# Optimization experiments

Measured on AMD Instinct MI355X. Metric: run time of the kernel, lower is better.

## Reference

```python
import jax, jax.numpy as jnp
import numpy as np

D_MODEL = 1024
N_HEADS = 16
HIDDEN = 256
PER_HEAD = 256
EPS = 1e-6


def setup_inputs() -> dict:
    key = jax.random.key(0)
    ks = jax.random.split(key, 6)
    B = 1024
    x = jax.random.normal(ks[0], (B, 64, D_MODEL), dtype=jnp.float32)
    # token_compress: Linear(d_model, 32, bias=False) -> weight (32, d_model)
    W_tc = jax.random.normal(ks[1], (32, D_MODEL), dtype=jnp.float32) / np.sqrt(D_MODEL)
    # global_compress: Linear(64*32, hidden) with bias, then RMSNorm(hidden)
    W_gc = jax.random.normal(ks[2], (HIDDEN, 64 * 32), dtype=jnp.float32) / np.sqrt(64 * 32)
    b_gc = jnp.zeros((HIDDEN,), dtype=jnp.float32)
    rms_scale = jnp.ones((HIDDEN,), dtype=jnp.float32)
    # per-head projections stacked: (n_heads, per_head, hidden)
    W_heads = jax.random.normal(ks[3], (N_HEADS, PER_HEAD, HIDDEN), dtype=jnp.float32) / np.sqrt(HIDDEN)
    # attn_logit_proj: Linear(per_head, 64*64, bias=False) -> (4096, per_head)
    W_logit = jax.random.normal(ks[4], (64 * 64, PER_HEAD), dtype=jnp.float32) / np.sqrt(PER_HEAD)
    return {"x": x, "W_tc": W_tc, "W_gc": W_gc, "b_gc": b_gc,
            "rms_scale": rms_scale, "W_heads": W_heads, "W_logit": W_logit}


def reference(x, W_tc, W_gc, b_gc, rms_scale, W_heads, W_logit):
    B = x.shape[0]
    # token compress: (B, 64, d_model) -> (B, 64, 32)
    compressed = jnp.einsum('bsd,kd->bsk', x, W_tc)
    flat = compressed.reshape(B, 64 * 32)
    # global compress + RMSNorm
    g = flat @ W_gc.T + b_gc                      # (B, hidden)
    rms = jnp.sqrt(jnp.mean(g * g, axis=-1, keepdims=True) + EPS)
    g = g / rms * rms_scale
    # batched per-head projection: (B, n_heads, per_head)
    head_repr = jnp.einsum('bh,nph->bnp', g, W_heads)
    # shared attn logit projection: (B, n_heads, 4096)
    logits = jnp.einsum('bnp,qp->bnq', head_repr, W_logit)
    return logits.reshape(B, N_HEADS, 64, 64)
```

## Files before the change

### kernel.cpp

```cpp
#include <hip/hip_runtime.h>


typedef unsigned short ushort_t;
typedef __attribute__((ext_vector_type(8))) short bf16x8;
typedef __attribute__((ext_vector_type(4))) float f32x4;
typedef __attribute__((ext_vector_type(4))) unsigned int u32x4;
typedef __attribute__((ext_vector_type(2))) unsigned int u32x2;

#define MFMA16(a, b, c) __builtin_amdgcn_mfma_f32_16x16x32_bf16((a), (b), (c), 0, 0, 0)

__device__ __forceinline__ unsigned bfround(float f) {
  unsigned u = __builtin_bit_cast(unsigned, f);
  return u + 0x7fffu + ((u >> 16) & 1u);
}
__device__ __forceinline__ unsigned pack2(float lo, float hi) {
  return (bfround(lo) >> 16) | (bfround(hi) & 0xffff0000u);
}

__device__ __forceinline__ void gld16(const ushort_t* g, ushort_t* l) {
  __builtin_amdgcn_global_load_lds(
      (const __attribute__((address_space(1))) unsigned int*)g,
      (__attribute__((address_space(3))) unsigned int*)l, 16, 0, 0);
}

__global__ __launch_bounds__(256) void k_cvt(const float* __restrict__ Wtc,
                                             const float* __restrict__ Wgc,
                                             const float* __restrict__ Wh,
                                             const float* __restrict__ Wl,
                                             ushort_t* __restrict__ oTc,
                                             ushort_t* __restrict__ oGc,
                                             ushort_t* __restrict__ oWh,
                                             ushort_t* __restrict__ oWl) {
  size_t g = (size_t)blockIdx.x * 256 + threadIdx.x;
  const float* src; ushort_t* dst; size_t off;
  if (g < 4096)        { src = Wtc; dst = oTc; off = g; }
  else if (g < 69632)  { src = Wgc; dst = oGc; off = g - 4096; }
  else if (g < 200704) { src = Wh;  dst = oWh; off = g - 69632; }
  else                 { src = Wl;  dst = oWl; off = g - 200704; }
  float4 f0 = ((const float4*)src)[off * 2];
  float4 f1 = ((const float4*)src)[off * 2 + 1];
  u32x4 p;
  p.x = pack2(f0.x, f0.y); p.y = pack2(f0.z, f0.w);
  p.z = pack2(f1.x, f1.y); p.w = pack2(f1.z, f1.w);
  ((u32x4*)dst)[off] = p;
}

__global__ __launch_bounds__(256) void k_tok(const float* __restrict__ x,
                                             const ushort_t* __restrict__ WtcBf,
                                             ushort_t* __restrict__ flatBf) {
  __shared__ ushort_t lb[32][264];
  const int t = threadIdx.x;
  const int w = t >> 6, l = t & 63, col16 = l & 15, quad = l >> 4;
  const float* arow = x + (size_t)blockIdx.x * 65536 + (size_t)(w * 16 + col16) * 1024;
  f32x4 acc0 = {0.f, 0.f, 0.f, 0.f}, acc1 = {0.f, 0.f, 0.f, 0.f};

  for (int ko = 0; ko < 1024; ko += 256) {
    float4 af[16];
#pragma unroll
    for (int s = 0; s < 8; ++s) {
      af[2 * s]     = *(const float4*)(arow + ko + s * 32 + quad * 8);
      af[2 * s + 1] = *(const float4*)(arow + ko + s * 32 + quad * 8 + 4);
    }
    __syncthreads();
    {
      int r = t >> 3, c0 = (t & 7) * 32;
      const ushort_t* src = WtcBf + (size_t)r * 1024 + ko + c0;
#pragma unroll
      for (int c = 0; c < 4; ++c)
        *(bf16x8*)&lb[r][c0 + c * 8] = *(const bf16x8*)(src + c * 8);
    }
    __syncthreads();
#pragma unroll
    for (int s = 0; s < 8; ++s) {
      u32x4 p;
      p.x = pack2(af[2 * s].x, af[2 * s].y);
      p.y = pack2(af[2 * s].z, af[2 * s].w);
      p.z = pack2(af[2 * s + 1].x, af[2 * s + 1].y);
      p.w = pack2(af[2 * s + 1].z, af[2 * s + 1].w);
      bf16x8 a = __builtin_bit_cast(bf16x8, p);
      bf16x8 b0 = *(const bf16x8*)&lb[col16][s * 32 + quad * 8];
      bf16x8 b1 = *(const bf16x8*)&lb[16 + col16][s * 32 + quad * 8];
      acc0 = MFMA16(b0, a, acc0);
      acc1 = MFMA16(b1, a, acc1);
    }
  }
  ushort_t* ob = flatBf + (size_t)blockIdx.x * 2048;
  const int m = w * 16 + col16;
  u32x2 v0, v1;
  v0.x = pack2(acc0[0], acc0[1]); v0.y = pack2(acc0[2], acc0[3]);
  v1.x = pack2(acc1[0], acc1[1]); v1.y = pack2(acc1[2], acc1[3]);
  *(u32x2*)&ob[m * 32 + quad * 4] = v0;
  *(u32x2*)&ob[m * 32 + 16 + quad * 4] = v1;
}

__global__ __launch_bounds__(256) void k_gc_part(const ushort_t* __restrict__ Abf,
                                                 const ushort_t* __restrict__ Bbf,
                                                 float* __restrict__ Hpart) {
  __shared__ ushort_t la[16][40];
  __shared__ ushort_t lb[256][40];
  const int t = threadIdx.x;
  const int w = t >> 6, l = t & 63, col16 = l & 15, quad = l >> 4;
  const int b0 = blockIdx.x * 16;
  const int k0 = blockIdx.y * 512;
  f32x4 acc[4];
#pragma unroll
  for (int j = 0; j < 4; ++j) acc[j] = (f32x4){0.f, 0.f, 0.f, 0.f};

  for (int kk = 0; kk < 512; kk += 32) {
    __syncthreads();
    if (t < 128) {
      int r = t >> 3, c0 = (t & 7) * 4;
      *(ushort4*)&la[r][c0] =
          *(const ushort4*)(Abf + (size_t)(b0 + r) * 2048 + k0 + kk + c0);
    }
    {
      const ushort_t* src = Bbf + (size_t)t * 2048 + k0 + kk;
#pragma unroll
      for (int c = 0; c < 4; ++c)
        *(bf16x8*)&lb[t][c * 8] = *(const bf16x8*)(src + c * 8);
    }
    __syncthreads();
    bf16x8 af = *(const bf16x8*)&la[col16][quad * 8];
#pragma unroll
    for (int j = 0; j < 4; ++j) {
      bf16x8 bfj = *(const bf16x8*)&lb[w * 64 + j * 16 + col16][quad * 8];
      acc[j] = MFMA16(bfj, af, acc[j]);
    }
  }
  float* o = Hpart + (size_t)blockIdx.y * 262144;
#pragma unroll
  for (int j = 0; j < 4; ++j)
    *(f32x4*)&o[(size_t)(b0 + col16) * 256 + w * 64 + j * 16 + quad * 4] = acc[j];
}

__global__ __launch_bounds__(256) void k_gc_red(const float* __restrict__ Hpart,
                                                const float* __restrict__ bias,
                                                const float* __restrict__ rscale,
                                                ushort_t* __restrict__ gBf) {
  __shared__ float lred[16][17];
  __shared__ float linv[16];
  const int t = threadIdx.x;
  const int row = t >> 4, seg = t & 15;
  const size_t base = (size_t)(blockIdx.x * 16 + row) * 256 + seg * 16;
  float v[16];
#pragma unroll
  for (int k = 0; k < 4; ++k) {
    float4 s0 = *(const float4*)(Hpart + base + k * 4);
    float4 s1 = *(const float4*)(Hpart + 262144 + base + k * 4);
    float4 s2 = *(const float4*)(Hpart + 524288 + base + k * 4);
    float4 s3 = *(const float4*)(Hpart + 786432 + base + k * 4);
    float4 bi = *(const float4*)(bias + seg * 16 + k * 4);
    v[k * 4 + 0] = s0.x + s1.x + s2.x + s3.x + bi.x;
    v[k * 4 + 1] = s0.y + s1.y + s2.y + s3.y + bi.y;
    v[k * 4 + 2] = s0.z + s1.z + s2.z + s3.z + bi.z;
    v[k * 4 + 3] = s0.w + s1.w + s2.w + s3.w + bi.w;
  }
  float ss = 0.f;
#pragma unroll
  for (int k = 0; k < 16; ++k) ss += v[k] * v[k];
  lred[row][seg] = ss;
  __syncthreads();
  if (t < 16) {
    float s = 0.f;
#pragma unroll
    for (int k = 0; k < 16; ++k) s += lred[t][k];
    linv[t] = 1.0f / sqrtf(s * (1.0f / 256.0f) + 1e-6f);
  }
  __syncthreads();
  float iv = linv[row];
  float rs[16];
#pragma unroll
  for (int k = 0; k < 4; ++k)
    *(float4*)&rs[k * 4] = *(const float4*)(rscale + seg * 16 + k * 4);
  u32x4 p0, p1;
  p0.x = pack2(v[0] * iv * rs[0],  v[1] * iv * rs[1]);
  p0.y = pack2(v[2] * iv * rs[2],  v[3] * iv * rs[3]);
  p0.z = pack2(v[4] * iv * rs[4],  v[5] * iv * rs[5]);
  p0.w = pack2(v[6] * iv * rs[6],  v[7] * iv * rs[7]);
  p1.x = pack2(v[8] * iv * rs[8],  v[9] * iv * rs[9]);
  p1.y = pack2(v[10] * iv * rs[10], v[11] * iv * rs[11]);
  p1.z = pack2(v[12] * iv * rs[12], v[13] * iv * rs[13]);
  p1.w = pack2(v[14] * iv * rs[14], v[15] * iv * rs[15]);
  *(u32x4*)(gBf + base) = p0;
  *(u32x4*)(gBf + base + 8) = p1;
}

template <bool OBF>
__global__ __launch_bounds__(256) void k_gemm(const ushort_t* __restrict__ A,
                                              const ushort_t* __restrict__ Bw,
                                              float* __restrict__ Cf,
                                              ushort_t* __restrict__ Cb) {
  __shared__ ushort_t la[2][4096];
  __shared__ ushort_t lb[2][4096];
  const int t = threadIdx.x;
  const int w = t >> 6, l = t & 63, col16 = l & 15, quad = l >> 4;
  const int wm = w >> 1, wn = w & 1;
  const int id = blockIdx.x;
  const int id2 = (id & 7) * ((int)gridDim.x >> 3) + (id >> 3);
  const size_t am0 = (size_t)(id2 >> 5) * 128;
  const size_t bn0 = (size_t)(id2 & 31) * 128;

  f32x4 acc[4][4];
#pragma unroll
  for (int i = 0; i < 4; ++i)
#pragma unroll
    for (int j = 0; j < 4; ++j) acc[i][j] = (f32x4){0.f, 0.f, 0.f, 0.f};

  auto STAGE = [&](int buf, int kk) {
#pragma unroll
    for (int i = 0; i < 2; ++i) {
      int L = i * 256 + t;
      int r = L >> 2;
      int cs = (L & 3) ^ (r & 3);
      ushort_t* da = &la[buf][(size_t)(i * 256 + (w << 6)) * 8];
      ushort_t* db = &lb[buf][(size_t)(i * 256 + (w << 6)) * 8];
      gld16(A + (am0 + r) * 256 + kk + cs * 8, da);
      gld16(Bw + (bn0 + r) * 256 + kk + cs * 8, db);
    }
  };

  STAGE(0, 0);
  __syncthreads();
#pragma unroll
  for (int tix = 0; tix < 8; ++tix) {
    const int buf = tix & 1;
    if (tix < 7) STAGE(buf ^ 1, (tix + 1) * 32);
    bf16x8 af[4], bfv[4];
#pragma unroll
    for (int i = 0; i < 4; ++i) {
      int R = wm * 64 + i * 16 + col16;
      af[i] = *(const bf16x8*)&la[buf][(size_t)((R << 2) + (quad ^ (R & 3))) * 8];
    }
#pragma unroll
    for (int j = 0; j < 4; ++j) {
      int R = wn * 64 + j * 16 + col16;
      bfv[j] = *(const bf16x8*)&lb[buf][(size_t)((R << 2) + (quad ^ (R & 3))) * 8];
    }
#pragma unroll
    for (int i = 0; i < 4; ++i)
#pragma unroll
      for (int j = 0; j < 4; ++j)
        acc[i][j] = MFMA16(bfv[j], af[i], acc[i][j]);
    __syncthreads();
  }

#pragma unroll
  for (int i = 0; i < 4; ++i)
#pragma unroll
    for (int j = 0; j < 4; ++j) {
      size_t row = am0 + wm * 64 + i * 16 + col16;
      size_t cc = bn0 + wn * 64 + j * 16 + quad * 4;
      if (OBF) {
        u32x2 v;
        v.x = pack2(acc[i][j][0], acc[i][j][1]);
        v.y = pack2(acc[i][j][2], acc[i][j][3]);
        *(u32x2*)&Cb[row * 4096 + cc] = v;
      } else {
        *(f32x4*)&Cf[row * 4096 + cc] = acc[i][j];
      }
    }
}

extern "C" void kernel_launch(void* const* d_in, const int* in_sizes, int n_in,
                              void* d_out, int out_size, void* d_ws, size_t ws_size,
                              hipStream_t stream) {
  const float* x   = (const float*)d_in[0];
  const float* Wtc = (const float*)d_in[1];
  const float* Wgc = (const float*)d_in[2];
  const float* bgc = (const float*)d_in[3];
  const float* rsc = (const float*)d_in[4];
  const float* Wh  = (const float*)d_in[5];
  const float* Wl  = (const float*)d_in[6];
  float* out = (float*)d_out;

  char* ws = (char*)d_ws;
  ushort_t* oTc    = (ushort_t*)(ws);
  ushort_t* oGc    = (ushort_t*)(ws + 65536);
  ushort_t* oWh    = (ushort_t*)(ws + 1114112);
  ushort_t* oWl    = (ushort_t*)(ws + 3211264);
  ushort_t* flatBf = (ushort_t*)(ws + 5308416);
  ushort_t* gBf    = (ushort_t*)(ws + 9502720);
  ushort_t* HBf    = (ushort_t*)(ws + 10027008);
  float*    Hpart  = (float*)(ws + 18415616);

  k_cvt<<<1296, 256, 0, stream>>>(Wtc, Wgc, Wh, Wl, oTc, oGc, oWh, oWl);
  k_tok<<<1024, 256, 0, stream>>>(x, oTc, flatBf);
  k_gc_part<<<dim3(64, 4), 256, 0, stream>>>(flatBf, oGc, Hpart);
  k_gc_red<<<64, 256, 0, stream>>>(Hpart, bgc, rsc, gBf);
  k_gemm<true><<<256, 256, 0, stream>>>(gBf, oWh, nullptr, HBf);
  k_gemm<false><<<4096, 256, 0, stream>>>(HBf, oWl, out, nullptr);
}
```

Baseline: 524.0 us.

## Fuse global-compress split-K with RMSNorm, stream x and output nontemporally

Merges the split-K global-compress GEMM and its reduction/RMSNorm kernel into a single kernel that runs the full K range with register prefetch, removing the fp32 partial buffer round-trip and one launch. The token-compress kernel drops its LDS staging and barriers, reading weight fragments directly from global memory and streaming x with nontemporal loads. The final logits GEMM writes output with nontemporal stores. The fused gc kernel launches only 64 blocks, so that stage has less parallelism.

```diff
diff --git a/kernel.cpp b/kernel.cpp
--- a/kernel.cpp
+++ b/kernel.cpp
@@ -15,6 +15,9 @@
 }
 __device__ __forceinline__ unsigned pack2(float lo, float hi) {
   return (bfround(lo) >> 16) | (bfround(hi) & 0xffff0000u);
+}
+__device__ __forceinline__ f32x4 ldnt4(const float* p) {
+  return __builtin_nontemporal_load((const f32x4*)p);
 }
 
 __device__ __forceinline__ void gld16(const ushort_t* g, ushort_t* l) {
@@ -48,41 +51,26 @@
 __global__ __launch_bounds__(256) void k_tok(const float* __restrict__ x,
                                              const ushort_t* __restrict__ WtcBf,
                                              ushort_t* __restrict__ flatBf) {
-  __shared__ ushort_t lb[32][264];
   const int t = threadIdx.x;
   const int w = t >> 6, l = t & 63, col16 = l & 15, quad = l >> 4;
-  const float* arow = x + (size_t)blockIdx.x * 65536 + (size_t)(w * 16 + col16) * 1024;
+  const float* arow =
+      x + (size_t)blockIdx.x * 65536 + (size_t)(w * 16 + col16) * 1024 + quad * 8;
+  const ushort_t* wr0 = WtcBf + (size_t)col16 * 1024 + quad * 8;
+  const ushort_t* wr1 = WtcBf + (size_t)(16 + col16) * 1024 + quad * 8;
   f32x4 acc0 = {0.f, 0.f, 0.f, 0.f}, acc1 = {0.f, 0.f, 0.f, 0.f};
 
-  for (int ko = 0; ko < 1024; ko += 256) {
-    float4 af[16];
-#pragma unroll
-    for (int s = 0; s < 8; ++s) {
-      af[2 * s]     = *(const float4*)(arow + ko + s * 32 + quad * 8);
-      af[2 * s + 1] = *(const float4*)(arow + ko + s * 32 + quad * 8 + 4);
-    }
-    __syncthreads();
-    {
-      int r = t >> 3, c0 = (t & 7) * 32;
-      const ushort_t* src = WtcBf + (size_t)r * 1024 + ko + c0;
-#pragma unroll
-      for (int c = 0; c < 4; ++c)
-        *(bf16x8*)&lb[r][c0 + c * 8] = *(const bf16x8*)(src + c * 8);
-    }
-    __syncthreads();
-#pragma unroll
-    for (int s = 0; s < 8; ++s) {
-      u32x4 p;
-      p.x = pack2(af[2 * s].x, af[2 * s].y);
-      p.y = pack2(af[2 * s].z, af[2 * s].w);
-      p.z = pack2(af[2 * s + 1].x, af[2 * s + 1].y);
-      p.w = pack2(af[2 * s + 1].z, af[2 * s + 1].w);
-      bf16x8 a = __builtin_bit_cast(bf16x8, p);
-      bf16x8 b0 = *(const bf16x8*)&lb[col16][s * 32 + quad * 8];
-      bf16x8 b1 = *(const bf16x8*)&lb[16 + col16][s * 32 + quad * 8];
-      acc0 = MFMA16(b0, a, acc0);
-      acc1 = MFMA16(b1, a, acc1);
-    }
+#pragma unroll 8
+  for (int k0 = 0; k0 < 1024; k0 += 32) {
+    f32x4 f0 = ldnt4(arow + k0);
+    f32x4 f1 = ldnt4(arow + k0 + 4);
+    bf16x8 b0 = *(const bf16x8*)(wr0 + k0);
+    bf16x8 b1 = *(const bf16x8*)(wr1 + k0);
+    u32x4 p;
+    p.x = pack2(f0.x, f0.y); p.y = pack2(f0.z, f0.w);
+    p.z = pack2(f1.x, f1.y); p.w = pack2(f1.z, f1.w);
+    bf16x8 a = __builtin_bit_cast(bf16x8, p);
+    acc0 = MFMA16(b0, a, acc0);
+    acc1 = MFMA16(b1, a, acc1);
   }
   ushort_t* ob = flatBf + (size_t)blockIdx.x * 2048;
   const int m = w * 16 + col16;
@@ -93,31 +81,43 @@
   *(u32x2*)&ob[m * 32 + 16 + quad * 4] = v1;
 }
 
-__global__ __launch_bounds__(256) void k_gc_part(const ushort_t* __restrict__ Abf,
-                                                 const ushort_t* __restrict__ Bbf,
-                                                 float* __restrict__ Hpart) {
+__global__ __launch_bounds__(256) void k_gc(const ushort_t* __restrict__ Abf,
+                                            const ushort_t* __restrict__ Bbf,
+                                            const float* __restrict__ bias,
+                                            const float* __restrict__ rscale,
+                                            ushort_t* __restrict__ gBf) {
   __shared__ ushort_t la[16][40];
   __shared__ ushort_t lb[256][40];
+  __shared__ float lred[16][17];
+  __shared__ float linv[16];
   const int t = threadIdx.x;
   const int w = t >> 6, l = t & 63, col16 = l & 15, quad = l >> 4;
   const int b0 = blockIdx.x * 16;
-  const int k0 = blockIdx.y * 512;
+  const int ar = t >> 3, ac0 = (t & 7) * 4;
   f32x4 acc[4];
 #pragma unroll
   for (int j = 0; j < 4; ++j) acc[j] = (f32x4){0.f, 0.f, 0.f, 0.f};
 
-  for (int kk = 0; kk < 512; kk += 32) {
+  ushort4 ra;
+  bf16x8 rb[4];
+  if (t < 128) ra = *(const ushort4*)(Abf + (size_t)(b0 + ar) * 2048 + ac0);
+  {
+    const ushort_t* src = Bbf + (size_t)t * 2048;
+#pragma unroll
+    for (int c = 0; c < 4; ++c) rb[c] = *(const bf16x8*)(src + c * 8);
+  }
+
+  for (int kk = 0; kk < 2048; kk += 32) {
     __syncthreads();
-    if (t < 128) {
-      int r = t >> 3, c0 = (t & 7) * 4;
-      *(ushort4*)&la[r][c0] =
-          *(const ushort4*)(Abf + (size_t)(b0 + r) * 2048 + k0 + kk + c0);
-    }
-    {
-      const ushort_t* src = Bbf + (size_t)t * 2048 + k0 + kk;
-#pragma unroll
-      for (int c = 0; c < 4; ++c)
-        *(bf16x8*)&lb[t][c * 8] = *(const bf16x8*)(src + c * 8);
+    if (t < 128) *(ushort4*)&la[ar][ac0] = ra;
+#pragma unroll
+    for (int c = 0; c < 4; ++c) *(bf16x8*)&lb[t][c * 8] = rb[c];
+    if (kk < 2016) {
+      const int kn = kk + 32;
+      if (t < 128) ra = *(const ushort4*)(Abf + (size_t)(b0 + ar) * 2048 + kn + ac0);
+      const ushort_t* src = Bbf + (size_t)t * 2048 + kn;
+#pragma unroll
+      for (int c = 0; c < 4; ++c) rb[c] = *(const bf16x8*)(src + c * 8);
     }
     __syncthreads();
     bf16x8 af = *(const bf16x8*)&la[col16][quad * 8];
@@ -127,38 +127,16 @@
       acc[j] = MFMA16(bfj, af, acc[j]);
     }
   }
-  float* o = Hpart + (size_t)blockIdx.y * 262144;
-#pragma unroll
-  for (int j = 0; j < 4; ++j)
-    *(f32x4*)&o[(size_t)(b0 + col16) * 256 + w * 64 + j * 16 + quad * 4] = acc[j];
-}
-
-__global__ __launch_bounds__(256) void k_gc_red(const float* __restrict__ Hpart,
-                                                const float* __restrict__ bias,
-                                                const float* __restrict__ rscale,
-                                                ushort_t* __restrict__ gBf) {
-  __shared__ float lred[16][17];
-  __shared__ float linv[16];
-  const int t = threadIdx.x;
-  const int row = t >> 4, seg = t & 15;
-  const size_t base = (size_t)(blockIdx.x * 16 + row) * 256 + seg * 16;
-  float v[16];
-#pragma unroll
-  for (int k = 0; k < 4; ++k) {
-    float4 s0 = *(const float4*)(Hpart + base + k * 4);
-    float4 s1 = *(const float4*)(Hpart + 262144 + base + k * 4);
-    float4 s2 = *(const float4*)(Hpart + 524288 + base + k * 4);
-    float4 s3 = *(const float4*)(Hpart + 786432 + base + k * 4);
-    float4 bi = *(const float4*)(bias + seg * 16 + k * 4);
-    v[k * 4 + 0] = s0.x + s1.x + s2.x + s3.x + bi.x;
-    v[k * 4 + 1] = s0.y + s1.y + s2.y + s3.y + bi.y;
-    v[k * 4 + 2] = s0.z + s1.z + s2.z + s3.z + bi.z;
-    v[k * 4 + 3] = s0.w + s1.w + s2.w + s3.w + bi.w;
-  }
+
   float ss = 0.f;
 #pragma unroll
-  for (int k = 0; k < 16; ++k) ss += v[k] * v[k];
-  lred[row][seg] = ss;
+  for (int j = 0; j < 4; ++j) {
+    float4 bi = *(const float4*)(bias + w * 64 + j * 16 + quad * 4);
+    acc[j][0] += bi.x; acc[j][1] += bi.y; acc[j][2] += bi.z; acc[j][3] += bi.w;
+    ss += acc[j][0] * acc[j][0] + acc[j][1] * acc[j][1] +
+          acc[j][2] * acc[j][2] + acc[j][3] * acc[j][3];
+  }
+  lred[col16][(w << 2) | quad] = ss;
   __syncthreads();
   if (t < 16) {
     float s = 0.f;
@@ -167,22 +145,15 @@
     linv[t] = 1.0f / sqrtf(s * (1.0f / 256.0f) + 1e-6f);
   }
   __syncthreads();
-  float iv = linv[row];
-  float rs[16];
-#pragma unroll
-  for (int k = 0; k < 4; ++k)
-    *(float4*)&rs[k * 4] = *(const float4*)(rscale + seg * 16 + k * 4);
-  u32x4 p0, p1;
-  p0.x = pack2(v[0] * iv * rs[0],  v[1] * iv * rs[1]);
-  p0.y = pack2(v[2] * iv * rs[2],  v[3] * iv * rs[3]);
-  p0.z = pack2(v[4] * iv * rs[4],  v[5] * iv * rs[5]);
-  p0.w = pack2(v[6] * iv * rs[6],  v[7] * iv * rs[7]);
-  p1.x = pack2(v[8] * iv * rs[8],  v[9] * iv * rs[9]);
-  p1.y = pack2(v[10] * iv * rs[10], v[11] * iv * rs[11]);
-  p1.z = pack2(v[12] * iv * rs[12], v[13] * iv * rs[13]);
-  p1.w = pack2(v[14] * iv * rs[14], v[15] * iv * rs[15]);
-  *(u32x4*)(gBf + base) = p0;
-  *(u32x4*)(gBf + base + 8) = p1;
+  const float iv = linv[col16];
+#pragma unroll
+  for (int j = 0; j < 4; ++j) {
+    float4 rs = *(const float4*)(rscale + w * 64 + j * 16 + quad * 4);
+    u32x2 v;
+    v.x = pack2(acc[j][0] * iv * rs.x, acc[j][1] * iv * rs.y);
+    v.y = pack2(acc[j][2] * iv * rs.z, acc[j][3] * iv * rs.w);
+    *(u32x2*)&gBf[(size_t)(b0 + col16) * 256 + w * 64 + j * 16 + quad * 4] = v;
+  }
 }
 
 template <bool OBF>
@@ -256,7 +227,7 @@
         v.y = pack2(acc[i][j][2], acc[i][j][3]);
         *(u32x2*)&Cb[row * 4096 + cc] = v;
       } else {
-        *(f32x4*)&Cf[row * 4096 + cc] = acc[i][j];
+        __builtin_nontemporal_store(acc[i][j], (f32x4*)&Cf[row * 4096 + cc]);
       }
     }
 }
@@ -281,12 +252,10 @@
   ushort_t* flatBf = (ushort_t*)(ws + 5308416);
   ushort_t* gBf    = (ushort_t*)(ws + 9502720);
   ushort_t* HBf    = (ushort_t*)(ws + 10027008);
-  float*    Hpart  = (float*)(ws + 18415616);
 
   k_cvt<<<1296, 256, 0, stream>>>(Wtc, Wgc, Wh, Wl, oTc, oGc, oWh, oWl);
   k_tok<<<1024, 256, 0, stream>>>(x, oTc, flatBf);
-  k_gc_part<<<dim3(64, 4), 256, 0, stream>>>(flatBf, oGc, Hpart);
-  k_gc_red<<<64, 256, 0, stream>>>(Hpart, bgc, rsc, gBf);
+  k_gc<<<64, 256, 0, stream>>>(flatBf, oGc, bgc, rsc, gBf);
   k_gemm<true><<<256, 256, 0, stream>>>(gBf, oWh, nullptr, HBf);
   k_gemm<false><<<4096, 256, 0, stream>>>(HBf, oWl, out, nullptr);
 }
```

After: 538.9 us. +2.8%, slower.
